# Performance work log

Measured on AMD Instinct MI355X. Metric: run time of the kernel, lower is better.

Reference implementation:

```python
import jax, jax.numpy as jnp
import numpy as np

# Irreps config: input/output = 32x0e + 16x1o (dim 80), H=4 heads -> head = 8x0e + 4x1o (dim 20)
M0, M1 = 32, 16      # input muls for 0e / 1o
m0, m1 = 8, 4        # per-head muls
H = 4
HEAD_DIM = m0 + 3 * m1   # 20
WNUM = H * (M0 * m0 + M1 * m0 + M0 * m1 + M1 * m1)  # 2304 per-edge TP weights
NB, HID = 16, 64
SQRT3 = np.float32(np.sqrt(3.0))
EPS = 1e-8


def radial_mlp(x, W1, b1, W2, b2):
    return jax.nn.silu(x @ W1 + b1) @ W2 + b2


def tp_edge(ss, vv, sh0, sh1, w):
    """FullyConnectedTensorProduct (32x0e+16x1o) x (1x0e+1x1o) -> H*(8x0e+4x1o) with per-edge weights w [E, WNUM].
    Paths: 0e*0e->0e, 1o*1o->0e (CG dot/sqrt3), 0e*1o->1o, 1o*0e->1o; path norm 1/sqrt(fan_in)."""
    E = ss.shape[0]
    per = M0 * m0 + M1 * m0 + M0 * m1 + M1 * m1  # 576
    w = w.reshape(E, H, per)
    o = 0
    Wss = w[..., o:o + M0 * m0].reshape(E, H, M0, m0); o += M0 * m0
    Wvv = w[..., o:o + M1 * m0].reshape(E, H, M1, m0); o += M1 * m0
    Wsv = w[..., o:o + M0 * m1].reshape(E, H, M0, m1); o += M0 * m1
    Wvs = w[..., o:o + M1 * m1].reshape(E, H, M1, m1)
    fan = np.float32(np.sqrt(M0 + M1))  # fan_in = 48 for both output irreps
    vv_dot = jnp.einsum('eui,ei->eu', vv, sh1) / SQRT3
    out0 = (jnp.einsum('eu,ehuw->ehw', ss * sh0[:, None], Wss)
            + jnp.einsum('eu,ehuw->ehw', vv_dot, Wvv)) / fan          # [E,H,m0]
    out1 = (jnp.einsum('eu,ehuw->ehw', ss, Wsv)[..., None] * sh1[:, None, None, :]
            + jnp.einsum('eui,ehuw->ehwi', vv * sh0[:, None, None], Wvs)) / fan  # [E,H,m1,3]
    return out0, out1


def setup_inputs() -> dict:
    key = jax.random.key(0)
    ks = jax.random.split(key, 24)
    N, E = 2000, 32000
    g = lambda k, s, sc=1.0: jax.random.normal(k, s, jnp.float32) * sc
    inp = {}
    inp['node_features'] = g(ks[0], (N, M0 + 3 * M1))
    inp['edge_index'] = jax.random.randint(ks[1], (2, E), 0, N)
    inp['edge_sh'] = g(ks[2], (E, 4))
    inp['edge_radial_emb'] = jax.random.uniform(ks[3], (E, NB), jnp.float32)
    # query e3nn Linear (per-head blocks)
    inp['Wq0'] = g(ks[4], (H, M0, m0))
    inp['Wq1'] = g(ks[5], (H, M1, m1))
    # radial MLPs for key / value TP weights
    inp['Wk1'] = g(ks[6], (NB, HID), 1 / np.sqrt(NB)); inp['bk1'] = jnp.zeros((HID,), jnp.float32)
    inp['Wk2'] = g(ks[7], (HID, WNUM), 1 / np.sqrt(HID)); inp['bk2'] = jnp.zeros((WNUM,), jnp.float32)
    inp['Wv1'] = g(ks[8], (NB, HID), 1 / np.sqrt(NB)); inp['bv1'] = jnp.zeros((HID,), jnp.float32)
    inp['Wv2'] = g(ks[9], (HID, WNUM), 1 / np.sqrt(HID)); inp['bv2'] = jnp.zeros((WNUM,), jnp.float32)
    # single-head dot-product TP -> 0e (shared weights)
    inp['Wd0'] = g(ks[10], (m0, m0))
    inp['Wd1'] = g(ks[11], (m1, m1))
    # output projection Linear (all heads mixed per irrep)
    inp['Wo0'] = g(ks[12], (H * m0, M0))
    inp['Wo1'] = g(ks[13], (H * m1, M1))
    # FFN: out irreps -> (2*M0)x0e + M1x1o -> out irreps
    inp['Wf1_0'] = g(ks[14], (M0, 2 * M0))
    inp['Wf1_1'] = g(ks[15], (M1, M1))
    inp['Wf2_0'] = g(ks[16], (2 * M0, M0))
    inp['Wf2_1'] = g(ks[17], (M1, M1))
    return inp


def reference(node_features, edge_index, edge_sh, edge_radial_emb,
              Wq0, Wq1, Wk1, bk1, Wk2, bk2, Wv1, bv1, Wv2, bv2,
              Wd0, Wd1, Wo0, Wo1, Wf1_0, Wf1_1, Wf2_0, Wf2_1):
    N = node_features.shape[0]
    s = node_features[:, :M0]                       # [N, M0] scalars
    v = node_features[:, M0:].reshape(N, M1, 3)     # [N, M1, 3] vectors
    src, dst = edge_index[0], edge_index[1]

    # query Linear (e3nn: per-irrep channel mix, norm 1/sqrt(fan_in))
    q0 = jnp.einsum('nu,huw->nhw', s, Wq0) / np.sqrt(M0)
    q1 = jnp.einsum('nui,huw->nhwi', v, Wq1) / np.sqrt(M1)

    sh0, sh1 = edge_sh[:, 0], edge_sh[:, 1:4]
    ss, vv = s[src], v[src]                         # gather per edge

    wk = radial_mlp(edge_radial_emb, Wk1, bk1, Wk2, bk2)
    wv = radial_mlp(edge_radial_emb, Wv1, bv1, Wv2, bv2)
    k0, k1 = tp_edge(ss, vv, sh0, sh1, wk)
    v0, v1 = tp_edge(ss, vv, sh0, sh1, wv)

    # per-head equivariant dot product -> 0e logits
    qd0, qd1 = q0[dst], q1[dst]
    fan_d = np.float32(np.sqrt(m0 * m0 + m1 * m1))
    logits = (jnp.einsum('ehu,uv,ehv->eh', qd0, Wd0, k0)
              + jnp.einsum('ehui,uv,ehvi->eh', qd1, Wd1, k1) / SQRT3) / fan_d
    logits = logits / np.sqrt(HEAD_DIM)             # self.scale
    logits = jnp.clip(logits, -10.0, 10.0)

    # scatter softmax over edges sharing a destination node
    seg_max = jax.ops.segment_max(logits, dst, num_segments=N)
    seg_max = jnp.maximum(seg_max, -10.0)           # handle empty segments
    ex = jnp.exp(logits - seg_max[dst])
    denom = jax.ops.segment_sum(ex, dst, num_segments=N)
    alpha = ex / (denom[dst] + 1e-12)               # [E, H]

    agg0 = jax.ops.segment_sum(alpha[..., None] * v0, dst, num_segments=N)        # [N,H,m0]
    agg1 = jax.ops.segment_sum(alpha[..., None, None] * v1, dst, num_segments=N)  # [N,H,m1,3]

    # output projection Linear over concatenated heads
    o0 = agg0.reshape(N, H * m0) @ Wo0 / np.sqrt(H * m0)
    o1 = jnp.einsum('nui,uw->nwi', agg1.reshape(N, H * m1, 3), Wo1) / np.sqrt(H * m1)

    # residual (input irreps == output irreps -> identity skip)
    x0 = s + o0
    x1 = v + o1

    # FFN with SafeNormActivation
    f0 = x0 @ Wf1_0 / np.sqrt(M0)                               # [N, 2*M0]
    f1 = jnp.einsum('nui,uw->nwi', x1, Wf1_1) / np.sqrt(M1)     # [N, M1, 3]
    a0 = jax.nn.silu(f0)
    norms = jnp.linalg.norm(f1, axis=-1, keepdims=True)
    safe = jnp.maximum(norms, EPS)
    a1 = jnp.where(norms < EPS, 0.0, (f1 / safe) * jax.nn.silu(norms))
    g0 = a0 @ Wf2_0 / np.sqrt(2 * M0)
    g1 = jnp.einsum('nui,uw->nwi', a1, Wf2_1) / np.sqrt(M1)

    out0 = x0 + g0
    out1 = x1 + g1
    return jnp.concatenate([out0, out1.reshape(N, M1 * 3)], axis=-1)
```

## Files before the change

### kernel.cpp

```cpp
#include <hip/hip_runtime.h>

typedef unsigned int uint;
typedef unsigned short ushort;
typedef __attribute__((ext_vector_type(8))) short bf16x8;
typedef __attribute__((ext_vector_type(4))) float f32x4;

#define N_NODES 2000
#define N_EDGES 32000
#define WNUM 2304

constexpr size_t OFF_AGG0 = 0;
constexpr size_t OFF_AGG1 = 64000;
constexpr size_t OFF_DEN  = 160000;
constexpr size_t OFF_FLAG = 168000;
constexpr size_t OFF_W2T  = 168004;
constexpr size_t OFF_QT0  = 315460;
constexpr size_t OFF_QT1  = 379460;
constexpr size_t OFF_CNT  = 475460;
constexpr size_t OFF_EORD = 477460;

__device__ __forceinline__ float b2f(ushort u){ union{uint i; float f;}x; x.i=((uint)u)<<16; return x.f; }
__device__ __forceinline__ float lo16(uint w){ union{uint u; float f;}x; x.u=w<<16; return x.f; }
__device__ __forceinline__ float hi16(uint w){ union{uint u; float f;}x; x.u=w&0xFFFF0000u; return x.f; }
__device__ __forceinline__ ushort f2b(float f){
  union{float f; uint u;}x; x.f=f;
  uint r = (x.u + 0x7FFFu + ((x.u>>16)&1u)) >> 16;
  return (ushort)r;
}
__device__ __forceinline__ float siluf(float x){ return x / (1.f + __expf(-x)); }

template<bool F32>
__device__ __forceinline__ float ldf(const void* p, int i){
  if (F32) return ((const float*)p)[i];
  return b2f(((const ushort*)p)[i]);
}
__device__ __forceinline__ float ldfr(const void* p, int i, bool f32){
  return f32 ? ((const float*)p)[i] : b2f(((const ushort*)p)[i]);
}

template<bool F32>
__device__ void node_q_one(const void* __restrict__ nf,
    const void* __restrict__ Wq0, const void* __restrict__ Wq1,
    const void* __restrict__ Wd0, const void* __restrict__ Wd1,
    float* __restrict__ qt0, float* __restrict__ qt1, int tid){
  int n = tid >> 2, h = tid & 3;
  float s[32], v[48];
  #pragma unroll
  for (int u=0; u<32; ++u) s[u] = ldf<F32>(nf, n*80+u);
  #pragma unroll
  for (int u=0; u<48; ++u) v[u] = ldf<F32>(nf, n*80+32+u);
  float q0[8];
  #pragma unroll
  for (int w=0; w<8; ++w){
    float a = 0.f;
    #pragma unroll
    for (int u=0; u<32; ++u) a += s[u]*ldf<F32>(Wq0, h*256 + u*8 + w);
    q0[w] = a * 0.17677669529663687f;
  }
  #pragma unroll
  for (int vv=0; vv<8; ++vv){
    float a = 0.f;
    #pragma unroll
    for (int u=0; u<8; ++u) a += q0[u]*ldf<F32>(Wd0, u*8+vv);
    qt0[n*32 + h*8 + vv] = a;
  }
  float q1[12];
  #pragma unroll
  for (int w=0; w<4; ++w)
    #pragma unroll
    for (int i=0; i<3; ++i){
      float a = 0.f;
      #pragma unroll
      for (int u=0; u<16; ++u) a += v[u*3+i]*ldf<F32>(Wq1, h*64 + u*4 + w);
      q1[w*3+i] = a * 0.25f;
    }
  #pragma unroll
  for (int vv=0; vv<4; ++vv)
    #pragma unroll
    for (int i=0; i<3; ++i){
      float a = 0.f;
      #pragma unroll
      for (int u=0; u<4; ++u) a += q1[u*3+i]*ldf<F32>(Wd1, u*4+vv);
      qt1[n*48 + h*12 + vv*3 + i] = a;
    }
}

__global__ __launch_bounds__(256) void prep_kernel(
    const void* __restrict__ nf, const void* __restrict__ Wk2, const void* __restrict__ Wv2,
    const void* __restrict__ Wq0, const void* __restrict__ Wq1,
    const void* __restrict__ Wd0, const void* __restrict__ Wd1,
    ushort* __restrict__ W2T, float* __restrict__ qt0, float* __restrict__ qt1,
    float* __restrict__ aggz, int* __restrict__ cnt, int* __restrict__ flag){
  __shared__ int s_cnt;
  const int t = threadIdx.x;
  if (t == 0) s_cnt = 0;
  __syncthreads();
  {
    uint u = ((const ushort*)nf)[t*2];
    uint ex = (u >> 7) & 0xFFu;
    if (ex >= 0xA0u) atomicAdd(&s_cnt, 1);
  }
  __syncthreads();
  const bool F32 = (s_cnt >= 20);
  if (blockIdx.x == 0 && t == 0) *flag = F32 ? 1 : 0;

  if (blockIdx.x < 72){
    __shared__ ushort tile[64][66];
    const int b = blockIdx.x, mat = b / 36, jt = b - mat*36;
    const void* W = mat ? Wv2 : Wk2;
    const int j0 = jt*64;
    const int jo = t & 63, cb = t >> 6;
    #pragma unroll
    for (int k=0; k<16; ++k){
      const int c = cb + k*4;
      tile[c][jo] = F32 ? f2b(((const float*)W)[(size_t)c*WNUM + j0 + jo])
                        : ((const ushort*)W)[(size_t)c*WNUM + j0 + jo];
    }
    __syncthreads();
    const int jl = t >> 2, c0 = (t & 3)*16;
    ushort* dst = W2T + (size_t)mat*147456 + (size_t)(j0+jl)*64 + c0;
    #pragma unroll
    for (int k=0; k<16; ++k) dst[k] = tile[c0+k][jl];
  } else {
    const int zb = (int)blockIdx.x - 72;
    float4* az = (float4*)aggz;
    for (int idx = zb*256 + t; idx < 42000; idx += 32*256)
      az[idx] = make_float4(0.f,0.f,0.f,0.f);
    for (int idx = zb*256 + t; idx < N_NODES; idx += 32*256)
      cnt[idx] = 0;
    const int tid = zb*256 + t;
    if (tid < N_NODES*4){
      if (F32) node_q_one<true >(nf, Wq0, Wq1, Wd0, Wd1, qt0, qt1, tid);
      else     node_q_one<false>(nf, Wq0, Wq1, Wd0, Wd1, qt0, qt1, tid);
    }
  }
}

__global__ __launch_bounds__(256) void cnt_kernel(const int* __restrict__ eidx, int* __restrict__ cnt){
  int e = blockIdx.x*256 + threadIdx.x;
  if (e < N_EDGES) atomicAdd(cnt + eidx[N_EDGES + e], 1);
}

__global__ __launch_bounds__(256) void scan_kernel(int* __restrict__ cnt){
  __shared__ int ls[256];
  const int t = threadIdx.x;
  const int base = t*8;
  int v[8]; int s = 0;
  #pragma unroll
  for (int k=0; k<8; ++k){ int idx = base+k; v[k] = (idx < N_NODES) ? cnt[idx] : 0; s += v[k]; }
  ls[t] = s; __syncthreads();
  for (int off=1; off<256; off<<=1){
    int x = (t >= off) ? ls[t-off] : 0;
    __syncthreads();
    ls[t] += x;
    __syncthreads();
  }
  int ex = ls[t] - s;
  #pragma unroll
  for (int k=0; k<8; ++k){ int idx = base+k; if (idx < N_NODES){ int c = v[k]; cnt[idx] = ex; ex += c; } }
}

__global__ __launch_bounds__(256) void scat_kernel(const int* __restrict__ eidx,
                                                   int* __restrict__ cnt, int* __restrict__ eord){
  int e = blockIdx.x*256 + threadIdx.x;
  if (e < N_EDGES){
    int p = atomicAdd(cnt + eidx[N_EDGES + e], 1);
    eord[p] = e;
  }
}

struct Smem {
  ushort hidA[2][32][72];
  float fssT[32][36];
  float fvvT[16][36];
  float sslT[32][36];
  float vshT[16][3][36];
  float sh1T[3][36];
  float cont[4][32][21];
  int   dstL[32];
};

template<bool F32>
__device__ void edge_body(
    const void* __restrict__ nf,  const int* __restrict__ eidx,
    const int* __restrict__ eord,
    const void* __restrict__ esh, const void* __restrict__ emb,
    const void* __restrict__ Wk1, const void* __restrict__ bk1, const void* __restrict__ bk2,
    const void* __restrict__ Wv1, const void* __restrict__ bv1, const void* __restrict__ bv2,
    const ushort* __restrict__ W2T,
    const float* __restrict__ qt0g, const float* __restrict__ qt1g,
    float* __restrict__ agg0, float* __restrict__ agg1, float* __restrict__ denom,
    Smem& sm){
  const int t  = threadIdx.x;
  const int hw = t >> 5;
  const int r  = t & 31;
  const int geb = blockIdx.x*32;

  #pragma unroll 1
  for (int e=0; e<4; ++e){
    const int le = hw*4+e;
    const int ge = eord[geb+le];
    const int src = eidx[ge], d = eidx[N_EDGES+ge];
    const float sh0 = ldf<F32>(esh, ge*4+0);
    const float s1a = ldf<F32>(esh, ge*4+1), s1b = ldf<F32>(esh, ge*4+2), s1c = ldf<F32>(esh, ge*4+3);
    if (r == 0) sm.dstL[le] = d;
    if (r < 3) sm.sh1T[r][le] = (r==0)? s1a : (r==1)? s1b : s1c;
    float sv = ldf<F32>(nf, src*80 + r);
    sm.sslT[r][le] = sv;
    sm.fssT[r][le] = sv * sh0;
    if (r < 16){
      float v0 = ldf<F32>(nf, src*80+32+r*3+0);
      float v1 = ldf<F32>(nf, src*80+32+r*3+1);
      float v2 = ldf<F32>(nf, src*80+32+r*3+2);
      sm.vshT[r][0][le] = v0*sh0; sm.vshT[r][1][le] = v1*sh0; sm.vshT[r][2][le] = v2*sh0;
      sm.fvvT[r][le] = (v0*s1a + v1*s1b + v2*s1c) * 0.5773502691896258f;
    }
  }

  #pragma unroll 1
  for (int e=0; e<4; ++e){
    const int le = hw*4+e;
    const int ge = eord[geb+le];
    float em[16];
    if (F32){
      const float4* p = (const float4*)((const float*)emb + ge*16);
      float4 a=p[0], b=p[1], c=p[2], d4=p[3];
      em[0]=a.x; em[1]=a.y; em[2]=a.z; em[3]=a.w;
      em[4]=b.x; em[5]=b.y; em[6]=b.z; em[7]=b.w;
      em[8]=c.x; em[9]=c.y; em[10]=c.z; em[11]=c.w;
      em[12]=d4.x; em[13]=d4.y; em[14]=d4.z; em[15]=d4.w;
    } else {
      const uint4* p = (const uint4*)((const ushort*)emb + ge*16);
      uint4 a=p[0], b=p[1];
      em[0]=lo16(a.x); em[1]=hi16(a.x); em[2]=lo16(a.y); em[3]=hi16(a.y);
      em[4]=lo16(a.z); em[5]=hi16(a.z); em[6]=lo16(a.w); em[7]=hi16(a.w);
      em[8]=lo16(b.x); em[9]=hi16(b.x); em[10]=lo16(b.y); em[11]=hi16(b.y);
      em[12]=lo16(b.z); em[13]=hi16(b.z); em[14]=lo16(b.w); em[15]=hi16(b.w);
    }
    #pragma unroll
    for (int cc=0; cc<2; ++cc){
      const int c = r + cc*32;
      float ak = ldf<F32>(bk1, c), av = ldf<F32>(bv1, c);
      #pragma unroll
      for (int b=0; b<16; ++b){
        ak += em[b] * ldf<F32>(Wk1, b*64 + c);
        av += em[b] * ldf<F32>(Wv1, b*64 + c);
      }
      sm.hidA[0][le][c] = f2b(siluf(ak));
      sm.hidA[1][le][c] = f2b(siluf(av));
    }
  }
  __syncthreads();

  const int h = t >> 6;
  const int lane = t & 63, q = lane >> 4, n = lane & 15;
  const ushort* w2tk = W2T;
  const ushort* w2tv = W2T + 147456;

  bf16x8 af[2][2][2];
  #pragma unroll
  for (int kv=0; kv<2; ++kv)
    #pragma unroll
    for (int Mt=0; Mt<2; ++Mt)
      #pragma unroll
      for (int kh=0; kh<2; ++kh)
        af[kv][Mt][kh] = *(const bf16x8*)&sm.hidA[kv][Mt*16+n][kh*32 + q*8];

  float aK0[2][4], aV0[2][4], aPK[2][4], aPV[2][4], aWK[3][2][4], aWV[3][2][4];
  #pragma unroll
  for (int Mt=0; Mt<2; ++Mt)
    #pragma unroll
    for (int z=0; z<4; ++z){
      aK0[Mt][z]=0.f; aV0[Mt][z]=0.f; aPK[Mt][z]=0.f; aPV[Mt][z]=0.f;
      aWK[0][Mt][z]=0.f; aWK[1][Mt][z]=0.f; aWK[2][Mt][z]=0.f;
      aWV[0][Mt][z]=0.f; aWV[1][Mt][z]=0.f; aWV[2][Mt][z]=0.f;
    }

  #pragma unroll 2
  for (int tl=0; tl<24; ++tl){
    const size_t tb = ((size_t)((h*36+tl)*16 + n))*64 + q*8;
    bf16x8 bk0 = *(const bf16x8*)(w2tk + tb), bk1f = *(const bf16x8*)(w2tk + tb + 32);
    bf16x8 bv0 = *(const bf16x8*)(w2tv + tb), bv1f = *(const bf16x8*)(w2tv + tb + 32);
    const int j = h*576 + tl*16 + n;
    const float bbk = ldf<F32>(bk2, j), bbv = ldf<F32>(bv2, j);
    const bool ss = (tl < 16);
    const int u = ss ? (tl*2 + (n>>3)) : ((tl-16)*2 + (n>>3));
    #pragma unroll
    for (int Mt=0; Mt<2; ++Mt){
      f32x4 fv = ss ? *(const f32x4*)&sm.fssT[u][Mt*16+q*4]
                    : *(const f32x4*)&sm.fvvT[u][Mt*16+q*4];
      f32x4 ck = {bbk,bbk,bbk,bbk};
      ck = __builtin_amdgcn_mfma_f32_16x16x32_bf16(af[0][Mt][0], bk0, ck, 0,0,0);
      ck = __builtin_amdgcn_mfma_f32_16x16x32_bf16(af[0][Mt][1], bk1f, ck, 0,0,0);
      f32x4 cv = {bbv,bbv,bbv,bbv};
      cv = __builtin_amdgcn_mfma_f32_16x16x32_bf16(af[1][Mt][0], bv0, cv, 0,0,0);
      cv = __builtin_amdgcn_mfma_f32_16x16x32_bf16(af[1][Mt][1], bv1f, cv, 0,0,0);
      #pragma unroll
      for (int z=0; z<4; ++z){ aK0[Mt][z] += ck[z]*fv[z]; aV0[Mt][z] += cv[z]*fv[z]; }
    }
  }
  #pragma unroll 2
  for (int tl=24; tl<32; ++tl){
    const size_t tb = ((size_t)((h*36+tl)*16 + n))*64 + q*8;
    bf16x8 bk0 = *(const bf16x8*)(w2tk + tb), bk1f = *(const bf16x8*)(w2tk + tb + 32);
    bf16x8 bv0 = *(const bf16x8*)(w2tv + tb), bv1f = *(const bf16x8*)(w2tv + tb + 32);
    const int j = h*576 + tl*16 + n;
    const float bbk = ldf<F32>(bk2, j), bbv = ldf<F32>(bv2, j);
    const int u = (tl-24)*4 + (n>>2);
    #pragma unroll
    for (int Mt=0; Mt<2; ++Mt){
      f32x4 fv = *(const f32x4*)&sm.sslT[u][Mt*16+q*4];
      f32x4 ck = {bbk,bbk,bbk,bbk};
      ck = __builtin_amdgcn_mfma_f32_16x16x32_bf16(af[0][Mt][0], bk0, ck, 0,0,0);
      ck = __builtin_amdgcn_mfma_f32_16x16x32_bf16(af[0][Mt][1], bk1f, ck, 0,0,0);
      f32x4 cv = {bbv,bbv,bbv,bbv};
      cv = __builtin_amdgcn_mfma_f32_16x16x32_bf16(af[1][Mt][0], bv0, cv, 0,0,0);
      cv = __builtin_amdgcn_mfma_f32_16x16x32_bf16(af[1][Mt][1], bv1f, cv, 0,0,0);
      #pragma unroll
      for (int z=0; z<4; ++z){ aPK[Mt][z] += ck[z]*fv[z]; aPV[Mt][z] += cv[z]*fv[z]; }
    }
  }
  #pragma unroll 1
  for (int tl=32; tl<36; ++tl){
    const size_t tb = ((size_t)((h*36+tl)*16 + n))*64 + q*8;
    bf16x8 bk0 = *(const bf16x8*)(w2tk + tb), bk1f = *(const bf16x8*)(w2tk + tb + 32);
    bf16x8 bv0 = *(const bf16x8*)(w2tv + tb), bv1f = *(const bf16x8*)(w2tv + tb + 32);
    const int j = h*576 + tl*16 + n;
    const float bbk = ldf<F32>(bk2, j), bbv = ldf<F32>(bv2, j);
    const int u = (tl-32)*4 + (n>>2);
    #pragma unroll
    for (int Mt=0; Mt<2; ++Mt){
      f32x4 ck = {bbk,bbk,bbk,bbk};
      ck = __builtin_amdgcn_mfma_f32_16x16x32_bf16(af[0][Mt][0], bk0, ck, 0,0,0);
      ck = __builtin_amdgcn_mfma_f32_16x16x32_bf16(af[0][Mt][1], bk1f, ck, 0,0,0);
      f32x4 cv = {bbv,bbv,bbv,bbv};
      cv = __builtin_amdgcn_mfma_f32_16x16x32_bf16(af[1][Mt][0], bv0, cv, 0,0,0);
      cv = __builtin_amdgcn_mfma_f32_16x16x32_bf16(af[1][Mt][1], bv1f, cv, 0,0,0);
      #pragma unroll
      for (int i=0; i<3; ++i){
        f32x4 fv = *(const f32x4*)&sm.vshT[u][i][Mt*16+q*4];
        #pragma unroll
        for (int z=0; z<4; ++z){ aWK[i][Mt][z] += ck[z]*fv[z]; aWV[i][Mt][z] += cv[z]*fv[z]; }
      }
    }
  }

  #pragma unroll
  for (int Mt=0; Mt<2; ++Mt)
    #pragma unroll
    for (int z=0; z<4; ++z){
      aK0[Mt][z] += __shfl_xor(aK0[Mt][z], 8, 64);
      aV0[Mt][z] += __shfl_xor(aV0[Mt][z], 8, 64);
      aPK[Mt][z] += __shfl_xor(aPK[Mt][z], 4, 64);
      aPK[Mt][z] += __shfl_xor(aPK[Mt][z], 8, 64);
      aPV[Mt][z] += __shfl_xor(aPV[Mt][z], 4, 64);
      aPV[Mt][z] += __shfl_xor(aPV[Mt][z], 8, 64);
      #pragma unroll
      for (int i=0; i<3; ++i){
        aWK[i][Mt][z] += __shfl_xor(aWK[i][Mt][z], 4, 64);
        aWK[i][Mt][z] += __shfl_xor(aWK[i][Mt][z], 8, 64);
        aWV[i][Mt][z] += __shfl_xor(aWV[i][Mt][z], 4, 64);
        aWV[i][Mt][z] += __shfl_xor(aWV[i][Mt][z], 8, 64);
      }
    }

  const float invfan = 0.14433756729740643f;
  int dn[2][4];
  #pragma unroll
  for (int Mt=0; Mt<2; ++Mt)
    #pragma unroll
    for (int z=0; z<4; ++z) dn[Mt][z] = sm.dstL[Mt*16 + q*4 + z];

  f32x4 s1v[3][2];
  #pragma unroll
  for (int i=0; i<3; ++i)
    #pragma unroll
    for (int Mt=0; Mt<2; ++Mt)
      s1v[i][Mt] = *(const f32x4*)&sm.sh1T[i][Mt*16+q*4];

  float lgp[2][4];
  #pragma unroll
  for (int Mt=0; Mt<2; ++Mt)
    #pragma unroll
    for (int z=0; z<4; ++z){
      float acc = 0.f;
      if (n < 8) acc = qt0g[dn[Mt][z]*32 + h*8 + n] * aK0[Mt][z];
      if (n < 4){
        float s = 0.f;
        #pragma unroll
        for (int i=0; i<3; ++i){
          float k1 = aPK[Mt][z]*s1v[i][Mt][z] + aWK[i][Mt][z];
          s += qt1g[dn[Mt][z]*48 + h*12 + n*3 + i] * k1;
        }
        acc += s * 0.5773502691896258f;
      }
      lgp[Mt][z] = acc;
    }
  #pragma unroll
  for (int Mt=0; Mt<2; ++Mt)
    #pragma unroll
    for (int z=0; z<4; ++z){
      lgp[Mt][z] += __shfl_xor(lgp[Mt][z], 1, 64);
      lgp[Mt][z] += __shfl_xor(lgp[Mt][z], 2, 64);
      lgp[Mt][z] += __shfl_xor(lgp[Mt][z], 4, 64);
      lgp[Mt][z] += __shfl_xor(lgp[Mt][z], 8, 64);
    }

  #pragma unroll
  for (int Mt=0; Mt<2; ++Mt)
    #pragma unroll
    for (int z=0; z<4; ++z){
      float lg = lgp[Mt][z] * invfan * 0.025f;
      lg = fminf(10.f, fmaxf(-10.f, lg));
      const float ex = __expf(lg - 10.0f);
      const int el = Mt*16 + q*4 + z;
      if (n == 0) sm.cont[h][el][0] = ex;
      if (n < 8)  sm.cont[h][el][1+n] = ex * aV0[Mt][z] * invfan;
      if (n < 4){
        #pragma unroll
        for (int i=0; i<3; ++i){
          float v1 = (aPV[Mt][z]*s1v[i][Mt][z] + aWV[i][Mt][z]) * invfan;
          sm.cont[h][el][9+n*3+i] = ex * v1;
        }
      }
    }
  __syncthreads();

  if (t < 84){
    const int h2 = t / 21, comp = t - h2*21;
    float acc = 0.f;
    #pragma unroll 1
    for (int e2=0; e2<32; ++e2){
      acc += sm.cont[h2][e2][comp];
      const int d2 = sm.dstL[e2];
      if (e2 == 31 || sm.dstL[e2+1] != d2){
        if (comp == 0)      atomicAdd(denom + d2*4  + h2, acc);
        else if (comp < 9)  atomicAdd(agg0  + d2*32 + h2*8  + (comp-1), acc);
        else                atomicAdd(agg1  + d2*48 + h2*12 + (comp-9), acc);
        acc = 0.f;
      }
    }
  }
}

__global__ __launch_bounds__(256) void edge_kernel(
    const void* nf, const int* eidx, const int* eord, const void* esh, const void* emb,
    const void* Wk1, const void* bk1, const void* bk2,
    const void* Wv1, const void* bv1, const void* bv2,
    const ushort* W2T, const float* qt0g, const float* qt1g,
    float* agg0, float* agg1, float* denom, const int* flag){
  __shared__ Smem sm;
  if (*flag)
    edge_body<true >(nf,eidx,eord,esh,emb,Wk1,bk1,bk2,Wv1,bv1,bv2,W2T,qt0g,qt1g,agg0,agg1,denom,sm);
  else
    edge_body<false>(nf,eidx,eord,esh,emb,Wk1,bk1,bk2,Wv1,bv1,bv2,W2T,qt0g,qt1g,agg0,agg1,denom,sm);
}

__global__ __launch_bounds__(64) void node_out_kernel(
    const void* __restrict__ nf, const float* __restrict__ agg0r, const float* __restrict__ agg1r,
    const float* __restrict__ denom,
    const void* __restrict__ Wo0, const void* __restrict__ Wo1,
    const void* __restrict__ Wf10, const void* __restrict__ Wf11,
    const void* __restrict__ Wf20, const void* __restrict__ Wf21,
    void* __restrict__ out, const int* __restrict__ flag){
  __shared__ float ag0[32], ag1[48], adiv[4];
  __shared__ float x0s[32], x1s[48], a0s[64], f1s[48], coefs[16];
  const bool F32 = (*flag) != 0;
  const int n = blockIdx.x, t = threadIdx.x;
  if (t < 4) adiv[t] = 1.f / (denom[n*4+t] + 1e-12f);
  __syncthreads();
  if (t < 32) ag0[t] = agg0r[n*32+t] * adiv[t>>3];
  if (t < 48) ag1[t] = agg1r[n*48+t] * adiv[t/12];
  __syncthreads();
  if (t < 32){
    float o = 0.f;
    #pragma unroll
    for (int k=0; k<32; ++k) o += ag0[k]*ldfr(Wo0, k*32+t, F32);
    x0s[t] = ldfr(nf, n*80+t, F32) + o*0.17677669529663687f;
  }
  if (t < 48){
    int w = t/3, i = t - w*3;
    float o = 0.f;
    #pragma unroll
    for (int u=0; u<16; ++u) o += ag1[u*3+i]*ldfr(Wo1, u*16+w, F32);
    x1s[t] = ldfr(nf, n*80+32+t, F32) + o*0.25f;
  }
  __syncthreads();
  {
    float f0 = 0.f;
    #pragma unroll
    for (int u=0; u<32; ++u) f0 += x0s[u]*ldfr(Wf10, u*64+t, F32);
    a0s[t] = siluf(f0*0.17677669529663687f);
  }
  if (t < 48){
    int w = t/3, i = t - w*3;
    float f1 = 0.f;
    #pragma unroll
    for (int u=0; u<16; ++u) f1 += x1s[u*3+i]*ldfr(Wf11, u*16+w, F32);
    f1s[t] = f1*0.25f;
  }
  __syncthreads();
  if (t < 16){
    float a = f1s[t*3], b = f1s[t*3+1], c = f1s[t*3+2];
    float nrm = sqrtf(a*a+b*b+c*c);
    float safe = fmaxf(nrm, 1e-8f);
    coefs[t] = (nrm < 1e-8f) ? 0.f : siluf(nrm)/safe;
  }
  __syncthreads();
  if (t < 32){
    float g = 0.f;
    #pragma unroll
    for (int u=0; u<64; ++u) g += a0s[u]*ldfr(Wf20, u*32+t, F32);
    float val = x0s[t] + g*0.125f;
    if (F32) ((float*)out)[n*80+t] = val; else ((ushort*)out)[n*80+t] = f2b(val);
  }
  if (t < 48){
    int w = t/3, i = t - w*3;
    float g = 0.f;
    #pragma unroll
    for (int u=0; u<16; ++u) g += coefs[u]*f1s[u*3+i]*ldfr(Wf21, u*16+w, F32);
    float val = x1s[t] + g*0.25f;
    if (F32) ((float*)out)[n*80+32+t] = val; else ((ushort*)out)[n*80+32+t] = f2b(val);
  }
}

extern "C" void kernel_launch(void* const* d_in, const int* in_sizes, int n_in,
                              void* d_out, int out_size, void* d_ws, size_t ws_size,
                              hipStream_t stream){
  const void* nf   = d_in[0];
  const int*  eidx = (const int*)d_in[1];
  const void* esh  = d_in[2];
  const void* emb  = d_in[3];
  const void* Wq0  = d_in[4];
  const void* Wq1  = d_in[5];
  const void* Wk1  = d_in[6];
  const void* bk1  = d_in[7];
  const void* Wk2  = d_in[8];
  const void* bk2  = d_in[9];
  const void* Wv1  = d_in[10];
  const void* bv1  = d_in[11];
  const void* Wv2  = d_in[12];
  const void* bv2  = d_in[13];
  const void* Wd0  = d_in[14];
  const void* Wd1  = d_in[15];
  const void* Wo0  = d_in[16];
  const void* Wo1  = d_in[17];
  const void* Wf10 = d_in[18];
  const void* Wf11 = d_in[19];
  const void* Wf20 = d_in[20];
  const void* Wf21 = d_in[21];
  float* ws = (float*)d_ws;

  float* agg0  = ws + OFF_AGG0;
  float* agg1  = ws + OFF_AGG1;
  float* denom = ws + OFF_DEN;
  int*   flag  = (int*)(ws + OFF_FLAG);
  ushort* W2T  = (ushort*)(ws + OFF_W2T);
  float* qt0   = ws + OFF_QT0;
  float* qt1   = ws + OFF_QT1;
  int*   cnt   = (int*)(ws + OFF_CNT);
  int*   eord  = (int*)(ws + OFF_EORD);

  prep_kernel<<<104, 256, 0, stream>>>(nf, Wk2, Wv2, Wq0, Wq1, Wd0, Wd1,
                                       W2T, qt0, qt1, agg0, cnt, flag);
  cnt_kernel<<<125, 256, 0, stream>>>(eidx, cnt);
  scan_kernel<<<1, 256, 0, stream>>>(cnt);
  scat_kernel<<<125, 256, 0, stream>>>(eidx, cnt, eord);
  edge_kernel<<<N_EDGES/32, 256, 0, stream>>>(nf, eidx, eord, esh, emb,
                                              Wk1, bk1, bk2, Wv1, bv1, bv2,
                                              W2T, qt0, qt1,
                                              agg0, agg1, denom, flag);
  node_out_kernel<<<N_NODES, 64, 0, stream>>>(nf, agg0, agg1, denom,
                                              Wo0, Wo1, Wf10, Wf11, Wf20, Wf21, d_out, flag);
}
```

Baseline: 239.3 us.

## Merge counting sort into one LDS kernel and serialize K/V edge MFMA passes

Replaces the three-kernel count/scan/scatter edge sort with a single 1024-thread block that histograms, scans and scatters in shared memory, removing two launches and global atomics. The edge kernel now processes the key and value weight matrices in sequential passes with fewer live accumulators. Partial results go to shared memory, and the logits, softmax numerators and value contributions are then computed from those shared-memory results. This cuts register pressure and may raise occupancy, at the cost of more LDS traffic, an extra barrier, and a single-block sort that runs on one CU.

```diff
diff --git a/kernel.cpp b/kernel.cpp
--- a/kernel.cpp
+++ b/kernel.cpp
@@ -16,8 +16,7 @@
 constexpr size_t OFF_W2T  = 168004;
 constexpr size_t OFF_QT0  = 315460;
 constexpr size_t OFF_QT1  = 379460;
-constexpr size_t OFF_CNT  = 475460;
-constexpr size_t OFF_EORD = 477460;
+constexpr size_t OFF_EORD = 475460;
 
 __device__ __forceinline__ float b2f(ushort u){ union{uint i; float f;}x; x.i=((uint)u)<<16; return x.f; }
 __device__ __forceinline__ float lo16(uint w){ union{uint u; float f;}x; x.u=w<<16; return x.f; }
@@ -90,7 +89,7 @@
     const void* __restrict__ Wq0, const void* __restrict__ Wq1,
     const void* __restrict__ Wd0, const void* __restrict__ Wd1,
     ushort* __restrict__ W2T, float* __restrict__ qt0, float* __restrict__ qt1,
-    float* __restrict__ aggz, int* __restrict__ cnt, int* __restrict__ flag){
+    float* __restrict__ aggz, int* __restrict__ flag){
   __shared__ int s_cnt;
   const int t = threadIdx.x;
   if (t == 0) s_cnt = 0;
@@ -126,8 +125,6 @@
     float4* az = (float4*)aggz;
     for (int idx = zb*256 + t; idx < 42000; idx += 32*256)
       az[idx] = make_float4(0.f,0.f,0.f,0.f);
-    for (int idx = zb*256 + t; idx < N_NODES; idx += 32*256)
-      cnt[idx] = 0;
     const int tid = zb*256 + t;
     if (tid < N_NODES*4){
       if (F32) node_q_one<true >(nf, Wq0, Wq1, Wd0, Wd1, qt0, qt1, tid);
@@ -136,35 +133,28 @@
   }
 }
 
-__global__ __launch_bounds__(256) void cnt_kernel(const int* __restrict__ eidx, int* __restrict__ cnt){
-  int e = blockIdx.x*256 + threadIdx.x;
-  if (e < N_EDGES) atomicAdd(cnt + eidx[N_EDGES + e], 1);
-}
-
-__global__ __launch_bounds__(256) void scan_kernel(int* __restrict__ cnt){
-  __shared__ int ls[256];
+__global__ __launch_bounds__(1024) void sort_kernel(const int* __restrict__ eidx,
+                                                    int* __restrict__ eord){
+  __shared__ int cnt[2048];
+  __shared__ int aux[1024];
   const int t = threadIdx.x;
-  const int base = t*8;
-  int v[8]; int s = 0;
-  #pragma unroll
-  for (int k=0; k<8; ++k){ int idx = base+k; v[k] = (idx < N_NODES) ? cnt[idx] : 0; s += v[k]; }
-  ls[t] = s; __syncthreads();
-  for (int off=1; off<256; off<<=1){
-    int x = (t >= off) ? ls[t-off] : 0;
+  cnt[t] = 0; cnt[t+1024] = 0;
+  __syncthreads();
+  for (int e=t; e<N_EDGES; e+=1024) atomicAdd(&cnt[eidx[N_EDGES+e]], 1);
+  __syncthreads();
+  int a = cnt[2*t], b = cnt[2*t+1], s = a+b;
+  aux[t] = s; __syncthreads();
+  for (int off=1; off<1024; off<<=1){
+    int x = (t>=off)? aux[t-off] : 0;
     __syncthreads();
-    ls[t] += x;
+    aux[t] += x;
     __syncthreads();
   }
-  int ex = ls[t] - s;
-  #pragma unroll
-  for (int k=0; k<8; ++k){ int idx = base+k; if (idx < N_NODES){ int c = v[k]; cnt[idx] = ex; ex += c; } }
-}
-
-__global__ __launch_bounds__(256) void scat_kernel(const int* __restrict__ eidx,
-                                                   int* __restrict__ cnt, int* __restrict__ eord){
-  int e = blockIdx.x*256 + threadIdx.x;
-  if (e < N_EDGES){
-    int p = atomicAdd(cnt + eidx[N_EDGES + e], 1);
+  int ex = aux[t] - s;
+  cnt[2*t] = ex; cnt[2*t+1] = ex + a;
+  __syncthreads();
+  for (int e=t; e<N_EDGES; e+=1024){
+    int p = atomicAdd(&cnt[eidx[N_EDGES+e]], 1);
     eord[p] = e;
   }
 }
@@ -176,7 +166,10 @@
   float sslT[32][36];
   float vshT[16][3][36];
   float sh1T[3][36];
-  float cont[4][32][21];
+  float res0[2][4][32][8];
+  float resP[2][4][32][4];
+  float resW[2][4][32][12];
+  float exL[4][32];
   int   dstL[32];
 };
 
@@ -254,176 +247,125 @@
 
   const int h = t >> 6;
   const int lane = t & 63, q = lane >> 4, n = lane & 15;
-  const ushort* w2tk = W2T;
-  const ushort* w2tv = W2T + 147456;
-
-  bf16x8 af[2][2][2];
-  #pragma unroll
-  for (int kv=0; kv<2; ++kv)
+
+  #pragma unroll 1
+  for (int kv=0; kv<2; ++kv){
+    const ushort* wmat = W2T + (size_t)kv*147456;
+    const void* bvec = kv ? bv2 : bk2;
+    bf16x8 af[2][2];
     #pragma unroll
     for (int Mt=0; Mt<2; ++Mt)
       #pragma unroll
       for (int kh=0; kh<2; ++kh)
-        af[kv][Mt][kh] = *(const bf16x8*)&sm.hidA[kv][Mt*16+n][kh*32 + q*8];
-
-  float aK0[2][4], aV0[2][4], aPK[2][4], aPV[2][4], aWK[3][2][4], aWV[3][2][4];
-  #pragma unroll
-  for (int Mt=0; Mt<2; ++Mt)
-    #pragma unroll
-    for (int z=0; z<4; ++z){
-      aK0[Mt][z]=0.f; aV0[Mt][z]=0.f; aPK[Mt][z]=0.f; aPV[Mt][z]=0.f;
-      aWK[0][Mt][z]=0.f; aWK[1][Mt][z]=0.f; aWK[2][Mt][z]=0.f;
-      aWV[0][Mt][z]=0.f; aWV[1][Mt][z]=0.f; aWV[2][Mt][z]=0.f;
-    }
-
-  #pragma unroll 2
-  for (int tl=0; tl<24; ++tl){
-    const size_t tb = ((size_t)((h*36+tl)*16 + n))*64 + q*8;
-    bf16x8 bk0 = *(const bf16x8*)(w2tk + tb), bk1f = *(const bf16x8*)(w2tk + tb + 32);
-    bf16x8 bv0 = *(const bf16x8*)(w2tv + tb), bv1f = *(const bf16x8*)(w2tv + tb + 32);
-    const int j = h*576 + tl*16 + n;
-    const float bbk = ldf<F32>(bk2, j), bbv = ldf<F32>(bv2, j);
-    const bool ss = (tl < 16);
-    const int u = ss ? (tl*2 + (n>>3)) : ((tl-16)*2 + (n>>3));
-    #pragma unroll
-    for (int Mt=0; Mt<2; ++Mt){
-      f32x4 fv = ss ? *(const f32x4*)&sm.fssT[u][Mt*16+q*4]
-                    : *(const f32x4*)&sm.fvvT[u][Mt*16+q*4];
-      f32x4 ck = {bbk,bbk,bbk,bbk};
-      ck = __builtin_amdgcn_mfma_f32_16x16x32_bf16(af[0][Mt][0], bk0, ck, 0,0,0);
-      ck = __builtin_amdgcn_mfma_f32_16x16x32_bf16(af[0][Mt][1], bk1f, ck, 0,0,0);
-      f32x4 cv = {bbv,bbv,bbv,bbv};
-      cv = __builtin_amdgcn_mfma_f32_16x16x32_bf16(af[1][Mt][0], bv0, cv, 0,0,0);
-      cv = __builtin_amdgcn_mfma_f32_16x16x32_bf16(af[1][Mt][1], bv1f, cv, 0,0,0);
-      #pragma unroll
-      for (int z=0; z<4; ++z){ aK0[Mt][z] += ck[z]*fv[z]; aV0[Mt][z] += cv[z]*fv[z]; }
-    }
-  }
-  #pragma unroll 2
-  for (int tl=24; tl<32; ++tl){
-    const size_t tb = ((size_t)((h*36+tl)*16 + n))*64 + q*8;
-    bf16x8 bk0 = *(const bf16x8*)(w2tk + tb), bk1f = *(const bf16x8*)(w2tk + tb + 32);
-    bf16x8 bv0 = *(const bf16x8*)(w2tv + tb), bv1f = *(const bf16x8*)(w2tv + tb + 32);
-    const int j = h*576 + tl*16 + n;
-    const float bbk = ldf<F32>(bk2, j), bbv = ldf<F32>(bv2, j);
-    const int u = (tl-24)*4 + (n>>2);
-    #pragma unroll
-    for (int Mt=0; Mt<2; ++Mt){
-      f32x4 fv = *(const f32x4*)&sm.sslT[u][Mt*16+q*4];
-      f32x4 ck = {bbk,bbk,bbk,bbk};
-      ck = __builtin_amdgcn_mfma_f32_16x16x32_bf16(af[0][Mt][0], bk0, ck, 0,0,0);
-      ck = __builtin_amdgcn_mfma_f32_16x16x32_bf16(af[0][Mt][1], bk1f, ck, 0,0,0);
-      f32x4 cv = {bbv,bbv,bbv,bbv};
-      cv = __builtin_amdgcn_mfma_f32_16x16x32_bf16(af[1][Mt][0], bv0, cv, 0,0,0);
-      cv = __builtin_amdgcn_mfma_f32_16x16x32_bf16(af[1][Mt][1], bv1f, cv, 0,0,0);
-      #pragma unroll
-      for (int z=0; z<4; ++z){ aPK[Mt][z] += ck[z]*fv[z]; aPV[Mt][z] += cv[z]*fv[z]; }
-    }
-  }
-  #pragma unroll 1
-  for (int tl=32; tl<36; ++tl){
-    const size_t tb = ((size_t)((h*36+tl)*16 + n))*64 + q*8;
-    bf16x8 bk0 = *(const bf16x8*)(w2tk + tb), bk1f = *(const bf16x8*)(w2tk + tb + 32);
-    bf16x8 bv0 = *(const bf16x8*)(w2tv + tb), bv1f = *(const bf16x8*)(w2tv + tb + 32);
-    const int j = h*576 + tl*16 + n;
-    const float bbk = ldf<F32>(bk2, j), bbv = ldf<F32>(bv2, j);
-    const int u = (tl-32)*4 + (n>>2);
-    #pragma unroll
-    for (int Mt=0; Mt<2; ++Mt){
-      f32x4 ck = {bbk,bbk,bbk,bbk};
-      ck = __builtin_amdgcn_mfma_f32_16x16x32_bf16(af[0][Mt][0], bk0, ck, 0,0,0);
-      ck = __builtin_amdgcn_mfma_f32_16x16x32_bf16(af[0][Mt][1], bk1f, ck, 0,0,0);
-      f32x4 cv = {bbv,bbv,bbv,bbv};
-      cv = __builtin_amdgcn_mfma_f32_16x16x32_bf16(af[1][Mt][0], bv0, cv, 0,0,0);
-      cv = __builtin_amdgcn_mfma_f32_16x16x32_bf16(af[1][Mt][1], bv1f, cv, 0,0,0);
+        af[Mt][kh] = *(const bf16x8*)&sm.hidA[kv][Mt*16+n][kh*32 + q*8];
+
+    {
+      f32x4 acc[2] = {{0.f,0.f,0.f,0.f},{0.f,0.f,0.f,0.f}};
+      #pragma unroll 2
+      for (int tl=0; tl<24; ++tl){
+        const size_t tb = ((size_t)((h*36+tl)*16 + n))*64 + q*8;
+        bf16x8 b0 = *(const bf16x8*)(wmat + tb), b1 = *(const bf16x8*)(wmat + tb + 32);
+        const float bb = ldf<F32>(bvec, h*576 + tl*16 + n);
+        const int u = (tl < 16) ? (tl*2 + (n>>3)) : ((tl-16)*2 + (n>>3));
+        #pragma unroll
+        for (int Mt=0; Mt<2; ++Mt){
+          f32x4 fv = (tl < 16) ? *(const f32x4*)&sm.fssT[u][Mt*16+q*4]
+                               : *(const f32x4*)&sm.fvvT[u][Mt*16+q*4];
+          f32x4 c = {bb,bb,bb,bb};
+          c = __builtin_amdgcn_mfma_f32_16x16x32_bf16(af[Mt][0], b0, c, 0,0,0);
+          c = __builtin_amdgcn_mfma_f32_16x16x32_bf16(af[Mt][1], b1, c, 0,0,0);
+          #pragma unroll
+          for (int z=0; z<4; ++z) acc[Mt][z] += c[z]*fv[z];
+        }
+      }
+      #pragma unroll
+      for (int Mt=0; Mt<2; ++Mt)
+        #pragma unroll
+        for (int z=0; z<4; ++z){
+          float v = acc[Mt][z];
+          v += __shfl_xor(v, 8, 64);
+          if (n < 8) sm.res0[kv][h][Mt*16+q*4+z][n] = v;
+        }
+    }
+    {
+      f32x4 acc[2] = {{0.f,0.f,0.f,0.f},{0.f,0.f,0.f,0.f}};
+      #pragma unroll 2
+      for (int tl=24; tl<32; ++tl){
+        const size_t tb = ((size_t)((h*36+tl)*16 + n))*64 + q*8;
+        bf16x8 b0 = *(const bf16x8*)(wmat + tb), b1 = *(const bf16x8*)(wmat + tb + 32);
+        const float bb = ldf<F32>(bvec, h*576 + tl*16 + n);
+        const int u = (tl-24)*4 + (n>>2);
+        #pragma unroll
+        for (int Mt=0; Mt<2; ++Mt){
+          f32x4 fv = *(const f32x4*)&sm.sslT[u][Mt*16+q*4];
+          f32x4 c = {bb,bb,bb,bb};
+          c = __builtin_amdgcn_mfma_f32_16x16x32_bf16(af[Mt][0], b0, c, 0,0,0);
+          c = __builtin_amdgcn_mfma_f32_16x16x32_bf16(af[Mt][1], b1, c, 0,0,0);
+          #pragma unroll
+          for (int z=0; z<4; ++z) acc[Mt][z] += c[z]*fv[z];
+        }
+      }
+      #pragma unroll
+      for (int Mt=0; Mt<2; ++Mt)
+        #pragma unroll
+        for (int z=0; z<4; ++z){
+          float v = acc[Mt][z];
+          v += __shfl_xor(v, 4, 64);
+          v += __shfl_xor(v, 8, 64);
+          if (n < 4) sm.resP[kv][h][Mt*16+q*4+z][n] = v;
+        }
+    }
+    #pragma unroll 1
+    for (int i=0; i<3; ++i){
+      f32x4 acc[2] = {{0.f,0.f,0.f,0.f},{0.f,0.f,0.f,0.f}};
+      #pragma unroll
+      for (int tl=32; tl<36; ++tl){
+        const size_t tb = ((size_t)((h*36+tl)*16 + n))*64 + q*8;
+        bf16x8 b0 = *(const bf16x8*)(wmat + tb), b1 = *(const bf16x8*)(wmat + tb + 32);
+        const float bb = ldf<F32>(bvec, h*576 + tl*16 + n);
+        const int u = (tl-32)*4 + (n>>2);
+        #pragma unroll
+        for (int Mt=0; Mt<2; ++Mt){
+          f32x4 fv = *(const f32x4*)&sm.vshT[u][i][Mt*16+q*4];
+          f32x4 c = {bb,bb,bb,bb};
+          c = __builtin_amdgcn_mfma_f32_16x16x32_bf16(af[Mt][0], b0, c, 0,0,0);
+          c = __builtin_amdgcn_mfma_f32_16x16x32_bf16(af[Mt][1], b1, c, 0,0,0);
+          #pragma unroll
+          for (int z=0; z<4; ++z) acc[Mt][z] += c[z]*fv[z];
+        }
+      }
+      #pragma unroll
+      for (int Mt=0; Mt<2; ++Mt)
+        #pragma unroll
+        for (int z=0; z<4; ++z){
+          float v = acc[Mt][z];
+          v += __shfl_xor(v, 4, 64);
+          v += __shfl_xor(v, 8, 64);
+          if (n < 4) sm.resW[kv][h][Mt*16+q*4+z][i*4+n] = v;
+        }
+    }
+  }
+  __syncthreads();
+
+  const float invfan = 0.14433756729740643f;
+  if (t < 128){
+    const int h2 = t >> 5, e2 = t & 31;
+    const int d = sm.dstL[e2];
+    float lg0 = 0.f;
+    #pragma unroll
+    for (int w=0; w<8; ++w) lg0 += qt0g[d*32 + h2*8 + w] * sm.res0[0][h2][e2][w];
+    float lg1 = 0.f;
+    #pragma unroll
+    for (int w4=0; w4<4; ++w4)
       #pragma unroll
       for (int i=0; i<3; ++i){
-        f32x4 fv = *(const f32x4*)&sm.vshT[u][i][Mt*16+q*4];
-        #pragma unroll
-        for (int z=0; z<4; ++z){ aWK[i][Mt][z] += ck[z]*fv[z]; aWV[i][Mt][z] += cv[z]*fv[z]; }
-      }
-    }
-  }
-
-  #pragma unroll
-  for (int Mt=0; Mt<2; ++Mt)
-    #pragma unroll
-    for (int z=0; z<4; ++z){
-      aK0[Mt][z] += __shfl_xor(aK0[Mt][z], 8, 64);
-      aV0[Mt][z] += __shfl_xor(aV0[Mt][z], 8, 64);
-      aPK[Mt][z] += __shfl_xor(aPK[Mt][z], 4, 64);
-      aPK[Mt][z] += __shfl_xor(aPK[Mt][z], 8, 64);
-      aPV[Mt][z] += __shfl_xor(aPV[Mt][z], 4, 64);
-      aPV[Mt][z] += __shfl_xor(aPV[Mt][z], 8, 64);
-      #pragma unroll
-      for (int i=0; i<3; ++i){
-        aWK[i][Mt][z] += __shfl_xor(aWK[i][Mt][z], 4, 64);
-        aWK[i][Mt][z] += __shfl_xor(aWK[i][Mt][z], 8, 64);
-        aWV[i][Mt][z] += __shfl_xor(aWV[i][Mt][z], 4, 64);
-        aWV[i][Mt][z] += __shfl_xor(aWV[i][Mt][z], 8, 64);
-      }
-    }
-
-  const float invfan = 0.14433756729740643f;
-  int dn[2][4];
-  #pragma unroll
-  for (int Mt=0; Mt<2; ++Mt)
-    #pragma unroll
-    for (int z=0; z<4; ++z) dn[Mt][z] = sm.dstL[Mt*16 + q*4 + z];
-
-  f32x4 s1v[3][2];
-  #pragma unroll
-  for (int i=0; i<3; ++i)
-    #pragma unroll
-    for (int Mt=0; Mt<2; ++Mt)
-      s1v[i][Mt] = *(const f32x4*)&sm.sh1T[i][Mt*16+q*4];
-
-  float lgp[2][4];
-  #pragma unroll
-  for (int Mt=0; Mt<2; ++Mt)
-    #pragma unroll
-    for (int z=0; z<4; ++z){
-      float acc = 0.f;
-      if (n < 8) acc = qt0g[dn[Mt][z]*32 + h*8 + n] * aK0[Mt][z];
-      if (n < 4){
-        float s = 0.f;
-        #pragma unroll
-        for (int i=0; i<3; ++i){
-          float k1 = aPK[Mt][z]*s1v[i][Mt][z] + aWK[i][Mt][z];
-          s += qt1g[dn[Mt][z]*48 + h*12 + n*3 + i] * k1;
-        }
-        acc += s * 0.5773502691896258f;
-      }
-      lgp[Mt][z] = acc;
-    }
-  #pragma unroll
-  for (int Mt=0; Mt<2; ++Mt)
-    #pragma unroll
-    for (int z=0; z<4; ++z){
-      lgp[Mt][z] += __shfl_xor(lgp[Mt][z], 1, 64);
-      lgp[Mt][z] += __shfl_xor(lgp[Mt][z], 2, 64);
-      lgp[Mt][z] += __shfl_xor(lgp[Mt][z], 4, 64);
-      lgp[Mt][z] += __shfl_xor(lgp[Mt][z], 8, 64);
-    }
-
-  #pragma unroll
-  for (int Mt=0; Mt<2; ++Mt)
-    #pragma unroll
-    for (int z=0; z<4; ++z){
-      float lg = lgp[Mt][z] * invfan * 0.025f;
-      lg = fminf(10.f, fmaxf(-10.f, lg));
-      const float ex = __expf(lg - 10.0f);
-      const int el = Mt*16 + q*4 + z;
-      if (n == 0) sm.cont[h][el][0] = ex;
-      if (n < 8)  sm.cont[h][el][1+n] = ex * aV0[Mt][z] * invfan;
-      if (n < 4){
-        #pragma unroll
-        for (int i=0; i<3; ++i){
-          float v1 = (aPV[Mt][z]*s1v[i][Mt][z] + aWV[i][Mt][z]) * invfan;
-          sm.cont[h][el][9+n*3+i] = ex * v1;
-        }
-      }
-    }
+        float k1 = sm.resP[0][h2][e2][w4]*sm.sh1T[i][e2] + sm.resW[0][h2][e2][i*4+w4];
+        lg1 += qt1g[d*48 + h2*12 + w4*3 + i] * k1;
+      }
+    float lg = (lg0 + lg1*0.5773502691896258f) * invfan * 0.025f;
+    lg = fminf(10.f, fmaxf(-10.f, lg));
+    sm.exL[h2][e2] = __expf(lg - 10.0f);
+  }
   __syncthreads();
 
   if (t < 84){
@@ -431,7 +373,15 @@
     float acc = 0.f;
     #pragma unroll 1
     for (int e2=0; e2<32; ++e2){
-      acc += sm.cont[h2][e2][comp];
+      const float ex = sm.exL[h2][e2];
+      float val;
+      if (comp == 0) val = ex;
+      else if (comp < 9) val = ex * sm.res0[1][h2][e2][comp-1] * invfan;
+      else {
+        const int j = comp-9, w4 = j/3, i = j - w4*3;
+        val = ex * (sm.resP[1][h2][e2][w4]*sm.sh1T[i][e2] + sm.resW[1][h2][e2][i*4+w4]) * invfan;
+      }
+      acc += val;
       const int d2 = sm.dstL[e2];
       if (e2 == 31 || sm.dstL[e2+1] != d2){
         if (comp == 0)      atomicAdd(denom + d2*4  + h2, acc);
@@ -558,14 +508,11 @@
   ushort* W2T  = (ushort*)(ws + OFF_W2T);
   float* qt0   = ws + OFF_QT0;
   float* qt1   = ws + OFF_QT1;
-  int*   cnt   = (int*)(ws + OFF_CNT);
   int*   eord  = (int*)(ws + OFF_EORD);
 
   prep_kernel<<<104, 256, 0, stream>>>(nf, Wk2, Wv2, Wq0, Wq1, Wd0, Wd1,
-                                       W2T, qt0, qt1, agg0, cnt, flag);
-  cnt_kernel<<<125, 256, 0, stream>>>(eidx, cnt);
-  scan_kernel<<<1, 256, 0, stream>>>(cnt);
-  scat_kernel<<<125, 256, 0, stream>>>(eidx, cnt, eord);
+                                       W2T, qt0, qt1, agg0, flag);
+  sort_kernel<<<1, 1024, 0, stream>>>(eidx, eord);
   edge_kernel<<<N_EDGES/32, 256, 0, stream>>>(nf, eidx, eord, esh, emb,
                                               Wk1, bk1, bk2, Wv1, bv1, bv2,
                                               W2T, qt0, qt1,
```

Result: slower. 253.6 us (+6.0%).
